# Optimization experiments

Measured on AMD Instinct MI355X. Metric: run time of the kernel, lower is better.

Reference implementation:

```python
import jax, jax.numpy as jnp
import numpy as np

ROWS, COLS = 256, 256
NUM_IMAGES, NUM_RBF = 16, 128


def setup_inputs() -> dict:
    key = jax.random.key(0)
    k1, k2, k3 = jax.random.split(key, 3)
    centers = jax.random.normal(k1, (NUM_IMAGES, NUM_RBF, 2), dtype=jnp.float32)
    covariances = jax.random.uniform(k2, (NUM_IMAGES, NUM_RBF, 3), dtype=jnp.float32)
    amplitudes = jax.random.normal(k3, (NUM_IMAGES, NUM_RBF, 1), dtype=jnp.float32)
    return {"centers": centers, "covariances": covariances, "amplitudes": amplitudes}


def _make_grid(rows, cols):
    # make_grid returns (c_grid, r_grid) i.e. (x, y); flatten to (P,)
    r = jnp.arange(rows, dtype=jnp.float32)
    c = jnp.arange(cols, dtype=jnp.float32)
    r_grid, c_grid = jnp.meshgrid(r, c, indexing="ij")
    return c_grid.ravel(), r_grid.ravel()


def reference(centers, covariances, amplitudes):
    x, y = _make_grid(ROWS, COLS)                 # (P,)
    cx = centers[..., 0][..., None]               # (N, K, 1)
    cy = centers[..., 1][..., None]
    sigma = jnp.exp(covariances[..., 0])          # log-width -> sigma, (N, K)
    inv_two_sig2 = 0.5 / (sigma * sigma)          # (N, K)
    d2 = (x - cx) ** 2 + (y - cy) ** 2            # (N, K, P)
    g = jnp.exp(-d2 * inv_two_sig2[..., None])    # (N, K, P)
    val = jnp.einsum("nkp,nk->np", g, amplitudes[..., 0])
    return jax.nn.sigmoid(val).reshape(NUM_IMAGES, ROWS, COLS)
```

## Files before the change

### kernel.cpp

```cpp
#include <hip/hip_runtime.h>

#define NIMG 16
#define NRBF 128
#define ROWS 256
#define COLS 256
#define PIX  (ROWS * COLS)
#define TPB  256
#define RPB  16
#define BLKS_PER_IMG (ROWS / RPB)
#define KC   64
#define KSTR 72

typedef _Float16 f16x8 __attribute__((ext_vector_type(8)));
typedef float    f32x4 __attribute__((ext_vector_type(4)));

__global__ __launch_bounds__(TPB) void rbf_mfma_kernel(
    const float* __restrict__ centers,
    const float* __restrict__ covariances,
    const float* __restrict__ amplitudes,
    float* __restrict__ out)
{
    __shared__ _Float16 gxT[COLS][KSTR];
    __shared__ _Float16 gaT[RPB][KSTR];
    __shared__ float2   pxs[NRBF];
    __shared__ float4   pya[NRBF];

    const int tid  = threadIdx.x;
    const int lane = tid & 63;
    const int wave = tid >> 6;
    const int img  = blockIdx.x >> 4;
    const int blk  = blockIdx.x & 15;
    const int rb   = blk * RPB;

    const float LOG2E = 1.4426950408889634f;

    if (tid < NRBF) {
        const int k = tid;
        const float cx = centers[(img * NRBF + k) * 2 + 0];
        const float cy = centers[(img * NRBF + k) * 2 + 1];
        const float c0 = covariances[(img * NRBF + k) * 3 + 0];
        const float a  = amplitudes[img * NRBF + k];
        const float s = 0.8493218002880190f * __builtin_amdgcn_exp2f(-c0 * LOG2E);
        pxs[k] = make_float2(-s * cx, s);
        pya[k] = make_float4(-s * cy, s, a, 0.0f);
    }

    const int n  = lane & 15;
    const int q  = lane >> 4;
    const int col0 = wave * 64;

    f32x4 acc0 = {0,0,0,0}, acc1 = {0,0,0,0}, acc2 = {0,0,0,0}, acc3 = {0,0,0,0};

    const float xf = (float)tid;
    const int   m1  = tid & 15;
    const int   k1  = (tid >> 4) * 4;
    const float yf  = (float)(rb + m1);

    for (int c = 0; c < 2; ++c) {
        const int kb_g = c * KC;
        __syncthreads();

#pragma unroll
        for (int k8 = 0; k8 < KC / 8; ++k8) {
            f16x8 h;
#pragma unroll
            for (int j = 0; j < 8; ++j) {
                const float2 p = pxs[kb_g + k8 * 8 + j];
                const float dx = fmaf(xf, p.y, p.x);
                h[j] = (_Float16)__builtin_amdgcn_exp2f(-dx * dx);
            }
            *(f16x8*)&gxT[tid][k8 * 8] = h;
        }
        {
            _Float16 h[4];
#pragma unroll
            for (int j = 0; j < 4; ++j) {
                const float4 p = pya[kb_g + k1 + j];
                const float dy = fmaf(yf, p.y, p.x);
                h[j] = (_Float16)(p.z * __builtin_amdgcn_exp2f(-dy * dy));
            }
            *(__attribute__((ext_vector_type(4))) _Float16*)&gaT[m1][k1] =
                *(__attribute__((ext_vector_type(4))) _Float16*)h;
        }
        __syncthreads();

#pragma unroll
        for (int kc = 0; kc < 2; ++kc) {
            const int kb = kc * 32 + q * 8;
            const f16x8 afr = *(const f16x8*)&gaT[n][kb];
            const f16x8 b0  = *(const f16x8*)&gxT[col0 +  0 + n][kb];
            const f16x8 b1  = *(const f16x8*)&gxT[col0 + 16 + n][kb];
            const f16x8 b2  = *(const f16x8*)&gxT[col0 + 32 + n][kb];
            const f16x8 b3  = *(const f16x8*)&gxT[col0 + 48 + n][kb];
            acc0 = __builtin_amdgcn_mfma_f32_16x16x32_f16(afr, b0, acc0, 0, 0, 0);
            acc1 = __builtin_amdgcn_mfma_f32_16x16x32_f16(afr, b1, acc1, 0, 0, 0);
            acc2 = __builtin_amdgcn_mfma_f32_16x16x32_f16(afr, b2, acc2, 0, 0, 0);
            acc3 = __builtin_amdgcn_mfma_f32_16x16x32_f16(afr, b3, acc3, 0, 0, 0);
        }
    }

#define SIG(v) __builtin_amdgcn_rcpf(1.0f + __builtin_amdgcn_exp2f(-(v) * LOG2E))
    float* base = out + img * PIX + rb * COLS + n + col0;
#pragma unroll
    for (int r = 0; r < 4; ++r) {
        float* rp = base + (q * 4 + r) * COLS;
        rp[0]  = SIG(acc0[r]);
        rp[16] = SIG(acc1[r]);
        rp[32] = SIG(acc2[r]);
        rp[48] = SIG(acc3[r]);
    }
#undef SIG
}

extern "C" void kernel_launch(void* const* d_in, const int* in_sizes, int n_in,
                              void* d_out, int out_size, void* d_ws, size_t ws_size,
                              hipStream_t stream) {
    const float* centers     = (const float*)d_in[0];
    const float* covariances = (const float*)d_in[1];
    const float* amplitudes  = (const float*)d_in[2];
    float* out = (float*)d_out;

    dim3 grid(NIMG * BLKS_PER_IMG);
    dim3 block(TPB);
    rbf_mfma_kernel<<<grid, block, 0, stream>>>(centers, covariances, amplitudes, out);
}
```

Measured before the change: 60.65 us.

## Switch to square 64x64 output tiles to balance separable exp work

Each block now covers a 64x64 pixel tile instead of a 16-row by 256-column strip, with the full K=128 staged in one pass. Previously each block computed 256x128 column exponentials plus 16x128 row exponentials; now it computes 64x128 of each. This cuts total exp work per block, since the column factors were recomputed by every strip. It also removes the two-chunk K loop and its extra barriers, at the cost of a different output store pattern (64-wide row segments).

```diff
diff --git a/kernel.cpp b/kernel.cpp
--- a/kernel.cpp
+++ b/kernel.cpp
@@ -6,10 +6,9 @@
 #define COLS 256
 #define PIX  (ROWS * COLS)
 #define TPB  256
-#define RPB  16
-#define BLKS_PER_IMG (ROWS / RPB)
-#define KC   64
-#define KSTR 72
+#define TILE 64
+#define TPI  16
+#define KSTR 136
 
 typedef _Float16 f16x8 __attribute__((ext_vector_type(8)));
 typedef float    f32x4 __attribute__((ext_vector_type(4)));
@@ -20,8 +19,8 @@
     const float* __restrict__ amplitudes,
     float* __restrict__ out)
 {
-    __shared__ _Float16 gxT[COLS][KSTR];
-    __shared__ _Float16 gaT[RPB][KSTR];
+    __shared__ _Float16 gxT[TILE][KSTR];
+    __shared__ _Float16 gaT[TILE][KSTR];
     __shared__ float2   pxs[NRBF];
     __shared__ float4   pya[NRBF];
 
@@ -29,8 +28,9 @@
     const int lane = tid & 63;
     const int wave = tid >> 6;
     const int img  = blockIdx.x >> 4;
-    const int blk  = blockIdx.x & 15;
-    const int rb   = blk * RPB;
+    const int tile = blockIdx.x & 15;
+    const int rb   = (tile >> 2) * TILE;
+    const int cb   = (tile & 3) * TILE;
 
     const float LOG2E = 1.4426950408889634f;
 
@@ -44,63 +44,52 @@
         pxs[k] = make_float2(-s * cx, s);
         pya[k] = make_float4(-s * cy, s, a, 0.0f);
     }
+    __syncthreads();
 
-    const int n  = lane & 15;
-    const int q  = lane >> 4;
-    const int col0 = wave * 64;
+    const int   cc  = tid & 63;
+    const int   kb0 = (tid >> 6) * 32;
+    const float xf  = (float)(cb + cc);
+    const float yf  = (float)(rb + cc);
+
+#pragma unroll
+    for (int k8 = 0; k8 < 4; ++k8) {
+        const int kb = kb0 + k8 * 8;
+        f16x8 hx, ha;
+#pragma unroll
+        for (int j = 0; j < 8; ++j) {
+            const float2 px = pxs[kb + j];
+            const float dx = fmaf(xf, px.y, px.x);
+            hx[j] = (_Float16)__builtin_amdgcn_exp2f(-dx * dx);
+            const float4 py = pya[kb + j];
+            const float dy = fmaf(yf, py.y, py.x);
+            ha[j] = (_Float16)(py.z * __builtin_amdgcn_exp2f(-dy * dy));
+        }
+        *(f16x8*)&gxT[cc][kb] = hx;
+        *(f16x8*)&gaT[cc][kb] = ha;
+    }
+    __syncthreads();
+
+    const int n = lane & 15;
+    const int q = lane >> 4;
 
     f32x4 acc0 = {0,0,0,0}, acc1 = {0,0,0,0}, acc2 = {0,0,0,0}, acc3 = {0,0,0,0};
 
-    const float xf = (float)tid;
-    const int   m1  = tid & 15;
-    const int   k1  = (tid >> 4) * 4;
-    const float yf  = (float)(rb + m1);
-
-    for (int c = 0; c < 2; ++c) {
-        const int kb_g = c * KC;
-        __syncthreads();
-
 #pragma unroll
-        for (int k8 = 0; k8 < KC / 8; ++k8) {
-            f16x8 h;
-#pragma unroll
-            for (int j = 0; j < 8; ++j) {
-                const float2 p = pxs[kb_g + k8 * 8 + j];
-                const float dx = fmaf(xf, p.y, p.x);
-                h[j] = (_Float16)__builtin_amdgcn_exp2f(-dx * dx);
-            }
-            *(f16x8*)&gxT[tid][k8 * 8] = h;
-        }
-        {
-            _Float16 h[4];
-#pragma unroll
-            for (int j = 0; j < 4; ++j) {
-                const float4 p = pya[kb_g + k1 + j];
-                const float dy = fmaf(yf, p.y, p.x);
-                h[j] = (_Float16)(p.z * __builtin_amdgcn_exp2f(-dy * dy));
-            }
-            *(__attribute__((ext_vector_type(4))) _Float16*)&gaT[m1][k1] =
-                *(__attribute__((ext_vector_type(4))) _Float16*)h;
-        }
-        __syncthreads();
-
-#pragma unroll
-        for (int kc = 0; kc < 2; ++kc) {
-            const int kb = kc * 32 + q * 8;
-            const f16x8 afr = *(const f16x8*)&gaT[n][kb];
-            const f16x8 b0  = *(const f16x8*)&gxT[col0 +  0 + n][kb];
-            const f16x8 b1  = *(const f16x8*)&gxT[col0 + 16 + n][kb];
-            const f16x8 b2  = *(const f16x8*)&gxT[col0 + 32 + n][kb];
-            const f16x8 b3  = *(const f16x8*)&gxT[col0 + 48 + n][kb];
-            acc0 = __builtin_amdgcn_mfma_f32_16x16x32_f16(afr, b0, acc0, 0, 0, 0);
-            acc1 = __builtin_amdgcn_mfma_f32_16x16x32_f16(afr, b1, acc1, 0, 0, 0);
-            acc2 = __builtin_amdgcn_mfma_f32_16x16x32_f16(afr, b2, acc2, 0, 0, 0);
-            acc3 = __builtin_amdgcn_mfma_f32_16x16x32_f16(afr, b3, acc3, 0, 0, 0);
-        }
+    for (int kc = 0; kc < 4; ++kc) {
+        const int kb = kc * 32 + q * 8;
+        const f16x8 afr = *(const f16x8*)&gaT[wave * 16 + n][kb];
+        const f16x8 b0  = *(const f16x8*)&gxT[ 0 + n][kb];
+        const f16x8 b1  = *(const f16x8*)&gxT[16 + n][kb];
+        const f16x8 b2  = *(const f16x8*)&gxT[32 + n][kb];
+        const f16x8 b3  = *(const f16x8*)&gxT[48 + n][kb];
+        acc0 = __builtin_amdgcn_mfma_f32_16x16x32_f16(afr, b0, acc0, 0, 0, 0);
+        acc1 = __builtin_amdgcn_mfma_f32_16x16x32_f16(afr, b1, acc1, 0, 0, 0);
+        acc2 = __builtin_amdgcn_mfma_f32_16x16x32_f16(afr, b2, acc2, 0, 0, 0);
+        acc3 = __builtin_amdgcn_mfma_f32_16x16x32_f16(afr, b3, acc3, 0, 0, 0);
     }
 
 #define SIG(v) __builtin_amdgcn_rcpf(1.0f + __builtin_amdgcn_exp2f(-(v) * LOG2E))
-    float* base = out + img * PIX + rb * COLS + n + col0;
+    float* base = out + img * PIX + (rb + wave * 16) * COLS + cb + n;
 #pragma unroll
     for (int r = 0; r < 4; ++r) {
         float* rp = base + (q * 4 + r) * COLS;
@@ -120,7 +109,7 @@
     const float* amplitudes  = (const float*)d_in[2];
     float* out = (float*)d_out;
 
-    dim3 grid(NIMG * BLKS_PER_IMG);
+    dim3 grid(NIMG * TPI);
     dim3 block(TPB);
     rbf_mfma_kernel<<<grid, block, 0, stream>>>(centers, covariances, amplitudes, out);
 }
```

New measurement: 59.47 us. No clear change (-1.9%).
